# Kernel tuning notes

Hardware: AMD Instinct MI355X
Metric: run time of the kernel (lower is better)

## Reference

```python
import jax, jax.numpy as jnp
import numpy as np

BETA = 0.05
KNN = 6
UL_ALPHA = 0.05
UL_BETA = 1.0


def setup_inputs() -> dict:
    key = jax.random.key(0)
    k1, k2, k3 = jax.random.split(key, 3)
    B, D, N = 256, 2048, 16384
    inputs = jax.random.normal(k1, (B, D), dtype=jnp.float32)
    em = jax.random.normal(k2, (N, D), dtype=jnp.float32)
    # exemplar memory rows are kept unit-norm by the update rule
    em = em / jnp.linalg.norm(em, axis=1, keepdims=True)
    targets = jax.random.randint(k3, (B,), 0, N, dtype=jnp.int64)
    return {"inputs": inputs, "em": em, "targets": targets, "epoch": 10}


def smooth_hot(logits, targets, em, k):
    # Vectorized k-reciprocal neighbor search (replaces the per-sample Python loop).
    m, n = logits.shape
    # index_sorted[:, :k] == top-k class indices per sample
    _, topk_idx = jax.lax.top_k(logits, k)            # [m, k]
    neigh = em[topk_idx]                               # [m, k, d]
    sims = jnp.einsum('mkd,nd->mkn', neigh, em)        # [m, k, n]
    _, neigh_topk = jax.lax.top_k(sims, k)             # [m, k, k]
    # neighbor j of sample i is reciprocal if anchor (top-1 of i) is in its top-k
    anchor = topk_idx[:, :1, None]                     # [m, 1, 1]
    recip = (neigh_topk == anchor).any(axis=-1)        # [m, k]
    weights = jnp.where(recip, 3.0 / k, 0.0).astype(logits.dtype)
    rows = jnp.arange(m)[:, None]
    onehot = jnp.zeros_like(logits).at[rows, topk_idx].set(weights)
    onehot = onehot.at[jnp.arange(m), targets].set(1.0)
    return onehot


def reference(inputs, em, targets, epoch):
    # ExemplarMemory.forward: similarity logits against the memory bank
    logits = (inputs @ em.T) / BETA                    # [B, N]
    # epoch >= 5 and knn > 0 branch (epoch=10)
    onehot = jax.lax.stop_gradient(
        smooth_hot(jax.lax.stop_gradient(logits), targets, em, KNN))
    logp = jax.nn.log_softmax(logits, axis=1)
    beta_loss = (-(onehot * logp).sum(axis=1)).mean()
    t_re = jnp.where(onehot == 0.0, jnp.float32(1e-4), onehot)
    alpha_loss = (-(jax.nn.softmax(logits, axis=1) * jnp.log(t_re)).sum(axis=1)).mean()
    return (UL_ALPHA * alpha_loss, UL_BETA * beta_loss)
```

## Files before the change

kernel.cpp:

```cpp
#include <hip/hip_runtime.h>
#include <math.h>

#define DIMK 2048
#define NEMB 16384
#define NB 256
#define NR2 1536
#define INV_BETA 20.0f
#define NEG_INF (-3.0e38f)

typedef short short8 __attribute__((ext_vector_type(8)));
typedef float f32x4 __attribute__((ext_vector_type(4)));
typedef const __attribute__((address_space(1))) unsigned int* gas_ptr;
typedef __attribute__((address_space(3))) unsigned int* las_ptr;

__device__ __forceinline__ void gl_lds16(const void* g, void* l) {
  __builtin_amdgcn_global_load_lds((gas_ptr)g, (las_ptr)l, 16, 0, 0);
}

__device__ __forceinline__ unsigned short f2bf(float f) {
  unsigned u = __float_as_uint(f);
  u += 0x7fffu + ((u >> 16) & 1u);
  return (unsigned short)(u >> 16);
}

__device__ __forceinline__ void ins6i(float x, int xi, float v[6], int vi[6]) {
  if (x > v[5] || (x == v[5] && xi < vi[5])) {
    v[5] = x; vi[5] = xi;
#pragma unroll
    for (int j = 5; j > 0; j--) {
      if (v[j] > v[j - 1] || (v[j] == v[j - 1] && vi[j] < vi[j - 1])) {
        float tv = v[j]; v[j] = v[j - 1]; v[j - 1] = tv;
        int ti = vi[j]; vi[j] = vi[j - 1]; vi[j - 1] = ti;
      }
    }
  }
}

__global__ __launch_bounds__(256) void cvt_kernel(const float* __restrict__ src,
                                                  unsigned short* __restrict__ dst, int n4) {
  int i = blockIdx.x * 256 + threadIdx.x;
  if (i < n4) {
    float4 f = ((const float4*)src)[i];
    ushort4 o;
    o.x = f2bf(f.x); o.y = f2bf(f.y); o.z = f2bf(f.z); o.w = f2bf(f.w);
    ((ushort4*)dst)[i] = o;
  }
}

template <int MODE>
__global__ __launch_bounds__(256, 4) void gemm_kernel(
    const unsigned short* __restrict__ Abase, const unsigned short* __restrict__ Bbase,
    const int* __restrict__ nidx, float* __restrict__ outC,
    const float* __restrict__ saIn, int* __restrict__ cntOut) {
  constexpr int MTILE = (MODE == 0) ? 64 : 128;
  constexpr int MI = 4;
  constexpr int NI = (MODE == 0) ? 2 : 4;
  constexpr int NSUB_A = MTILE / 16;
  constexpr int NSUB = NSUB_A + 8;
  constexpr int NA = NSUB / 4;
  constexpr int NK = DIMK / 32;

  __shared__ unsigned short st[3][NSUB * 512];
  __shared__ int rowIdxSh[128];
  __shared__ float saSh[128];
  __shared__ int cntSh[128];
  int t = threadIdx.x;
  int lane = t & 63, wave = t >> 6;
  int quad = lane >> 4, l16 = lane & 15;
  int wr = (MODE == 0) ? 0 : (wave >> 1);
  int wc = (MODE == 0) ? wave : (wave & 1);
  int bn = blockIdx.x, bm = blockIdx.y;

  if constexpr (MODE == 1) {
    if (t < 128) {
      rowIdxSh[t] = nidx[bm * 128 + t];
      saSh[t] = saIn[bm * 128 + t];
      cntSh[t] = 0;
    }
  }
  __syncthreads();

  const unsigned short* agp[NA];
  int soff[NA];
  {
    int seg = lane >> 4;
#pragma unroll
    for (int a = 0; a < NA; a++) {
      int s = wave + a * 4;
      const unsigned short* basep;
      size_t goff;
      if (s < NSUB_A) {
        int r = s * 16 + l16;
        int grow = (MODE == 0) ? (bm * MTILE + r) : rowIdxSh[r];
        basep = Abase;
        goff = (size_t)grow * DIMK;
      } else {
        int r = (s - NSUB_A) * 16 + l16;
        basep = Bbase;
        goff = (size_t)(bn * 128 + r) * DIMK;
      }
      agp[a] = basep + goff + seg * 8;
      soff[a] = s * 512;
    }
  }

  f32x4 acc[MI][NI];
#pragma unroll
  for (int mi = 0; mi < MI; mi++)
#pragma unroll
    for (int ni = 0; ni < NI; ni++) acc[mi][ni] = (f32x4)0.0f;

  int lo = lane * 8;

#pragma unroll
  for (int p = 0; p < 3; p++)
#pragma unroll
    for (int a = 0; a < NA; a++) gl_lds16(agp[a] + p * 32, &st[p][soff[a]]);

  int cur = 0;
  for (int k = 0; k < NK; k++) {
    if (k < NK - 2) {
      if constexpr (MODE == 0) asm volatile("s_waitcnt vmcnt(6)" ::: "memory");
      else                     asm volatile("s_waitcnt vmcnt(8)" ::: "memory");
    } else if (k == NK - 2) {
      if constexpr (MODE == 0) asm volatile("s_waitcnt vmcnt(3)" ::: "memory");
      else                     asm volatile("s_waitcnt vmcnt(4)" ::: "memory");
    } else {
      asm volatile("s_waitcnt vmcnt(0)" ::: "memory");
    }
    __builtin_amdgcn_s_barrier();
    asm volatile("" ::: "memory");

    const unsigned short* hb = &st[cur][0];
    short8 af[MI], bfv[NI];
#pragma unroll
    for (int mi = 0; mi < MI; mi++)
      af[mi] = *(const short8*)&hb[(wr * MI + mi) * 512 + lo];
#pragma unroll
    for (int ni = 0; ni < NI; ni++)
      bfv[ni] = *(const short8*)&hb[(NSUB_A + wc * NI + ni) * 512 + lo];

    asm volatile("s_waitcnt lgkmcnt(0)" ::: "memory");
    __builtin_amdgcn_s_barrier();
    asm volatile("" ::: "memory");

    if (k + 3 < NK) {
#pragma unroll
      for (int a = 0; a < NA; a++) gl_lds16(agp[a] + (k + 3) * 32, &st[cur][soff[a]]);
    }

#pragma unroll
    for (int mi = 0; mi < MI; mi++)
#pragma unroll
      for (int ni = 0; ni < NI; ni++)
        acc[mi][ni] =
            __builtin_amdgcn_mfma_f32_16x16x32_bf16(af[mi], bfv[ni], acc[mi][ni], 0, 0, 0);

    cur = (cur == 2) ? 0 : cur + 1;
  }

  if constexpr (MODE == 0) {
#pragma unroll
    for (int mi = 0; mi < MI; mi++) {
      int row = bm * MTILE + mi * 16 + quad * 4;
#pragma unroll
      for (int ni = 0; ni < NI; ni++) {
        int col = bn * 128 + wave * 32 + ni * 16 + l16;
#pragma unroll
        for (int rr = 0; rr < 4; rr++)
          outC[(size_t)(row + rr) * NEMB + col] = acc[mi][ni][rr] * INV_BETA;
      }
    }
  } else {
#pragma unroll
    for (int mi = 0; mi < MI; mi++) {
#pragma unroll
      for (int rr = 0; rr < 4; rr++) {
        int rloc = wr * 64 + mi * 16 + quad * 4 + rr;
        float s = saSh[rloc];
        int c = 0;
#pragma unroll
        for (int ni = 0; ni < NI; ni++) c += (acc[mi][ni][rr] > s) ? 1 : 0;
        c += __shfl_xor(c, 1, 64);
        c += __shfl_xor(c, 2, 64);
        c += __shfl_xor(c, 4, 64);
        c += __shfl_xor(c, 8, 64);
        if (l16 == 0) atomicAdd(&cntSh[rloc], c);
      }
    }
    __syncthreads();
    if (t < 128) atomicAdd(&cntOut[bm * 128 + t], cntSh[t]);
  }
}

__global__ __launch_bounds__(1024) void rowstats_kernel(
    const float* __restrict__ logits, float* __restrict__ topv,
    int* __restrict__ topi, float* __restrict__ lse) {
  int m = blockIdx.x, t = threadIdx.x;
  const float4* row4 = (const float4*)(logits + (size_t)m * NEMB);
  float v6[6]; int i6[6];
#pragma unroll
  for (int j = 0; j < 6; j++) { v6[j] = NEG_INF; i6[j] = 0x7fffffff; }
  float vals[16];
#pragma unroll
  for (int j = 0; j < 4; j++) {
    float4 f = row4[t + j * 1024];
    vals[j * 4 + 0] = f.x; vals[j * 4 + 1] = f.y;
    vals[j * 4 + 2] = f.z; vals[j * 4 + 3] = f.w;
  }
  float mx = vals[0];
#pragma unroll
  for (int r = 1; r < 16; r++) mx = fmaxf(mx, vals[r]);
  float sme = 0.f;
#pragma unroll
  for (int r = 0; r < 16; r++) sme += expf(vals[r] - mx);
#pragma unroll
  for (int j = 0; j < 4; j++) {
    int base = (t + j * 1024) * 4;
#pragma unroll
    for (int b = 0; b < 4; b++) ins6i(vals[j * 4 + b], base + b, v6, i6);
  }
  __shared__ float sv[1024 * 6]; __shared__ int si[1024 * 6];
  __shared__ float smx[1024], ssm[1024];
#pragma unroll
  for (int j = 0; j < 6; j++) { sv[t * 6 + j] = v6[j]; si[t * 6 + j] = i6[j]; }
  smx[t] = mx; ssm[t] = sme;
  __syncthreads();
  for (int s = 512; s > 0; s >>= 1) {
    if (t < s) {
      float mo = smx[t + s], lo = ssm[t + s];
      float mn = fmaxf(smx[t], mo);
      ssm[t] = ssm[t] * expf(smx[t] - mn) + lo * expf(mo - mn);
      smx[t] = mn;
#pragma unroll
      for (int j = 0; j < 6; j++) ins6i(sv[(t + s) * 6 + j], si[(t + s) * 6 + j], v6, i6);
#pragma unroll
      for (int j = 0; j < 6; j++) { sv[t * 6 + j] = v6[j]; si[t * 6 + j] = i6[j]; }
    }
    __syncthreads();
  }
  if (t == 0) {
    lse[m] = smx[0] + logf(ssm[0]);
#pragma unroll
    for (int j = 0; j < 6; j++) { topv[m * 6 + j] = v6[j]; topi[m * 6 + j] = i6[j]; }
  }
}

__global__ __launch_bounds__(256) void sa_kernel(const float* __restrict__ em,
                                                 const int* __restrict__ topi,
                                                 float* __restrict__ sa,
                                                 int* __restrict__ cnt) {
  int gid = blockIdx.x * 256 + threadIdx.x;
  int w = gid >> 6, lane = gid & 63;
  if (w >= NR2) return;
  if (lane == 1) cnt[w] = 0;
  int m = w / 6;
  int i = topi[w], a = topi[m * 6];
  const float* ei = em + (size_t)i * DIMK;
  const float* ea = em + (size_t)a * DIMK;
  float s = 0.f;
  for (int d = lane; d < DIMK; d += 64) s += ei[d] * ea[d];
#pragma unroll
  for (int off = 32; off > 0; off >>= 1) s += __shfl_down(s, off, 64);
  if (lane == 0) sa[w] = s;
}

__global__ __launch_bounds__(256) void final_kernel(
    const float* __restrict__ logits, const float* __restrict__ topv,
    const int* __restrict__ topi, const float* __restrict__ lse_arr,
    const int* __restrict__ cnt, const int* __restrict__ targets,
    float* __restrict__ out) {
  int m = threadIdx.x;
  float lse = lse_arr[m];
  int tgt = targets[m];
  float tl = logits[(size_t)m * NEMB + tgt];
  float beta = 0.f, Ps = 0.f, nbp = 0.f;
  bool tin = false;
#pragma unroll
  for (int k = 0; k < 6; k++) {
    int idx = topi[m * 6 + k]; float v = topv[m * 6 + k];
    float p = expf(v - lse);
    if (idx == tgt) { tin = true; beta += (lse - v); Ps += p; }
    else if (cnt[m * 6 + k] < 6) { beta += 0.5f * (lse - v); Ps += p; nbp += p; }
  }
  if (!tin) { beta += (lse - tl); Ps += expf(tl - lse); }
  float alpha = 9.2103404f * (1.f - Ps) + 0.6931472f * nbp;
  __shared__ float sA[256], sB2[256];
  sA[m] = alpha; sB2[m] = beta;
  __syncthreads();
  for (int s = 128; s > 0; s >>= 1) {
    if (m < s) { sA[m] += sA[m + s]; sB2[m] += sB2[m + s]; }
    __syncthreads();
  }
  if (m == 0) { out[0] = 0.05f * sA[0] / 256.f; out[1] = sB2[0] / 256.f; }
}

extern "C" void kernel_launch(void* const* d_in, const int* in_sizes, int n_in,
                              void* d_out, int out_size, void* d_ws, size_t ws_size,
                              hipStream_t stream) {
  const float* x = (const float*)d_in[0];
  const float* em = (const float*)d_in[1];
  const int* targets = (const int*)d_in[2];
  char* ws = (char*)d_ws;
  unsigned short* em_bf = (unsigned short*)ws;
  unsigned short* x_bf  = (unsigned short*)(ws + 67108864);
  float* logits = (float*)(ws + 68157440);
  int*   cnt    = (int*)  (ws + 84934656);
  float* topv   = (float*)(ws + 89653248);
  int*   topi   = (int*)  (ws + 89659392);
  float* lse    = (float*)(ws + 89665536);
  float* sa     = (float*)(ws + 89666560);

  cvt_kernel<<<dim3(32768), dim3(256), 0, stream>>>(em, em_bf, NEMB * DIMK / 4);
  cvt_kernel<<<dim3(512), dim3(256), 0, stream>>>(x, x_bf, NB * DIMK / 4);
  gemm_kernel<0><<<dim3(128, 4), dim3(256), 0, stream>>>(x_bf, em_bf, (const int*)nullptr,
                                                         logits, (const float*)nullptr,
                                                         (int*)nullptr);
  rowstats_kernel<<<dim3(256), dim3(1024), 0, stream>>>(logits, topv, topi, lse);
  sa_kernel<<<dim3(384), dim3(256), 0, stream>>>(em, topi, sa, cnt);
  gemm_kernel<1><<<dim3(128, 12), dim3(256), 0, stream>>>(em_bf, em_bf, topi,
                                                          (float*)nullptr, sa, cnt);
  final_kernel<<<dim3(1), dim3(256), 0, stream>>>(logits, topv, topi, lse, cnt, targets,
                                                  (float*)d_out);
}
```

Measured before the change: 487.1 us.

## Split GEMM template and retile neighbor-count GEMM to 256-row, 512-thread blocks

Splits the templated GEMM into a plain logits GEMM and a dedicated neighbor-similarity counting GEMM. The counting GEMM now uses 512-thread blocks covering 256 gathered rows by 128 columns, with a K step of 64 split into two halves. It also uses hand-scheduled ds_read_b128 loads interleaved with MFMA groups, s_setprio around the MFMAs and sched barriers. The goal is more operand reuse per LDS byte and better overlap of LDS reads with matrix math. The cost is much larger shared memory (about 144KB per block), which caps occupancy, plus fragile manual wait counts.

Result: faster. 471.0 us (-3.3%).

```diff
diff --git a/kernel.cpp b/kernel.cpp
--- a/kernel.cpp
+++ b/kernel.cpp
@@ -16,6 +16,20 @@
 __device__ __forceinline__ void gl_lds16(const void* g, void* l) {
   __builtin_amdgcn_global_load_lds((gas_ptr)g, (las_ptr)l, 16, 0, 0);
 }
+
+__device__ __forceinline__ short8 dsr(const void* p) {
+  short8 r;
+  asm volatile("ds_read_b128 %0, %1"
+               : "=&v"(r)
+               : "v"((const __attribute__((address_space(3))) unsigned short*)p));
+  return r;
+}
+
+#define LGKM0_FENCE                                          \
+  do {                                                       \
+    asm volatile("s_waitcnt lgkmcnt(0)" ::: "memory");       \
+    __builtin_amdgcn_sched_barrier(0);                       \
+  } while (0)
 
 __device__ __forceinline__ unsigned short f2bf(float f) {
   unsigned u = __float_as_uint(f);
@@ -47,38 +61,16 @@
   }
 }
 
-template <int MODE>
-__global__ __launch_bounds__(256, 4) void gemm_kernel(
+__global__ __launch_bounds__(256, 4) void gemm0_kernel(
     const unsigned short* __restrict__ Abase, const unsigned short* __restrict__ Bbase,
-    const int* __restrict__ nidx, float* __restrict__ outC,
-    const float* __restrict__ saIn, int* __restrict__ cntOut) {
-  constexpr int MTILE = (MODE == 0) ? 64 : 128;
-  constexpr int MI = 4;
-  constexpr int NI = (MODE == 0) ? 2 : 4;
-  constexpr int NSUB_A = MTILE / 16;
-  constexpr int NSUB = NSUB_A + 8;
-  constexpr int NA = NSUB / 4;
-  constexpr int NK = DIMK / 32;
-
+    float* __restrict__ outC) {
+  constexpr int MI = 4, NI = 2, NSUB_A = 4, NSUB = 12, NA = 3, NK = DIMK / 32;
   __shared__ unsigned short st[3][NSUB * 512];
-  __shared__ int rowIdxSh[128];
-  __shared__ float saSh[128];
-  __shared__ int cntSh[128];
   int t = threadIdx.x;
   int lane = t & 63, wave = t >> 6;
   int quad = lane >> 4, l16 = lane & 15;
-  int wr = (MODE == 0) ? 0 : (wave >> 1);
-  int wc = (MODE == 0) ? wave : (wave & 1);
+  int wc = wave;
   int bn = blockIdx.x, bm = blockIdx.y;
-
-  if constexpr (MODE == 1) {
-    if (t < 128) {
-      rowIdxSh[t] = nidx[bm * 128 + t];
-      saSh[t] = saIn[bm * 128 + t];
-      cntSh[t] = 0;
-    }
-  }
-  __syncthreads();
 
   const unsigned short* agp[NA];
   int soff[NA];
@@ -87,17 +79,14 @@
 #pragma unroll
     for (int a = 0; a < NA; a++) {
       int s = wave + a * 4;
+      size_t goff;
       const unsigned short* basep;
-      size_t goff;
       if (s < NSUB_A) {
-        int r = s * 16 + l16;
-        int grow = (MODE == 0) ? (bm * MTILE + r) : rowIdxSh[r];
         basep = Abase;
-        goff = (size_t)grow * DIMK;
+        goff = (size_t)(bm * 64 + s * 16 + l16) * DIMK;
       } else {
-        int r = (s - NSUB_A) * 16 + l16;
         basep = Bbase;
-        goff = (size_t)(bn * 128 + r) * DIMK;
+        goff = (size_t)(bn * 128 + (s - NSUB_A) * 16 + l16) * DIMK;
       }
       agp[a] = basep + goff + seg * 8;
       soff[a] = s * 512;
@@ -111,7 +100,6 @@
     for (int ni = 0; ni < NI; ni++) acc[mi][ni] = (f32x4)0.0f;
 
   int lo = lane * 8;
-
 #pragma unroll
   for (int p = 0; p < 3; p++)
 #pragma unroll
@@ -119,78 +107,199 @@
 
   int cur = 0;
   for (int k = 0; k < NK; k++) {
-    if (k < NK - 2) {
-      if constexpr (MODE == 0) asm volatile("s_waitcnt vmcnt(6)" ::: "memory");
-      else                     asm volatile("s_waitcnt vmcnt(8)" ::: "memory");
-    } else if (k == NK - 2) {
-      if constexpr (MODE == 0) asm volatile("s_waitcnt vmcnt(3)" ::: "memory");
-      else                     asm volatile("s_waitcnt vmcnt(4)" ::: "memory");
-    } else {
-      asm volatile("s_waitcnt vmcnt(0)" ::: "memory");
-    }
+    if (k < NK - 2)      asm volatile("s_waitcnt vmcnt(6)" ::: "memory");
+    else if (k == NK - 2) asm volatile("s_waitcnt vmcnt(3)" ::: "memory");
+    else                 asm volatile("s_waitcnt vmcnt(0)" ::: "memory");
     __builtin_amdgcn_s_barrier();
     asm volatile("" ::: "memory");
-
     const unsigned short* hb = &st[cur][0];
     short8 af[MI], bfv[NI];
 #pragma unroll
-    for (int mi = 0; mi < MI; mi++)
-      af[mi] = *(const short8*)&hb[(wr * MI + mi) * 512 + lo];
+    for (int mi = 0; mi < MI; mi++) af[mi] = *(const short8*)&hb[mi * 512 + lo];
 #pragma unroll
     for (int ni = 0; ni < NI; ni++)
       bfv[ni] = *(const short8*)&hb[(NSUB_A + wc * NI + ni) * 512 + lo];
-
     asm volatile("s_waitcnt lgkmcnt(0)" ::: "memory");
     __builtin_amdgcn_s_barrier();
     asm volatile("" ::: "memory");
-
     if (k + 3 < NK) {
 #pragma unroll
       for (int a = 0; a < NA; a++) gl_lds16(agp[a] + (k + 3) * 32, &st[cur][soff[a]]);
     }
-
 #pragma unroll
     for (int mi = 0; mi < MI; mi++)
 #pragma unroll
       for (int ni = 0; ni < NI; ni++)
         acc[mi][ni] =
             __builtin_amdgcn_mfma_f32_16x16x32_bf16(af[mi], bfv[ni], acc[mi][ni], 0, 0, 0);
-
     cur = (cur == 2) ? 0 : cur + 1;
   }
 
-  if constexpr (MODE == 0) {
-#pragma unroll
-    for (int mi = 0; mi < MI; mi++) {
-      int row = bm * MTILE + mi * 16 + quad * 4;
-#pragma unroll
-      for (int ni = 0; ni < NI; ni++) {
-        int col = bn * 128 + wave * 32 + ni * 16 + l16;
-#pragma unroll
-        for (int rr = 0; rr < 4; rr++)
-          outC[(size_t)(row + rr) * NEMB + col] = acc[mi][ni][rr] * INV_BETA;
-      }
-    }
-  } else {
-#pragma unroll
-    for (int mi = 0; mi < MI; mi++) {
-#pragma unroll
-      for (int rr = 0; rr < 4; rr++) {
-        int rloc = wr * 64 + mi * 16 + quad * 4 + rr;
-        float s = saSh[rloc];
-        int c = 0;
-#pragma unroll
-        for (int ni = 0; ni < NI; ni++) c += (acc[mi][ni][rr] > s) ? 1 : 0;
-        c += __shfl_xor(c, 1, 64);
-        c += __shfl_xor(c, 2, 64);
-        c += __shfl_xor(c, 4, 64);
-        c += __shfl_xor(c, 8, 64);
-        if (l16 == 0) atomicAdd(&cntSh[rloc], c);
-      }
-    }
-    __syncthreads();
-    if (t < 128) atomicAdd(&cntOut[bm * 128 + t], cntSh[t]);
-  }
+#pragma unroll
+  for (int mi = 0; mi < MI; mi++) {
+    int row = bm * 64 + mi * 16 + quad * 4;
+#pragma unroll
+    for (int ni = 0; ni < NI; ni++) {
+      int col = bn * 128 + wave * 32 + ni * 16 + l16;
+#pragma unroll
+      for (int rr = 0; rr < 4; rr++)
+        outC[(size_t)(row + rr) * NEMB + col] = acc[mi][ni][rr] * INV_BETA;
+    }
+  }
+}
+
+__global__ __launch_bounds__(512, 2) void gemm1_kernel(
+    const unsigned short* __restrict__ em_bf, const int* __restrict__ nidx,
+    const float* __restrict__ saIn, int* __restrict__ cntOut) {
+  __shared__ unsigned short st[3][2][24 * 512];
+  __shared__ int rowIdxSh[256];
+  __shared__ float saSh[256];
+  __shared__ int cntSh[256];
+  int t = threadIdx.x;
+  int lane = t & 63, wave = t >> 6;
+  int quad = lane >> 4, l16 = lane & 15;
+  int wr = wave >> 2, wc = wave & 3;
+  int bn = blockIdx.x, bm = blockIdx.y;
+
+  if (t < 256) {
+    rowIdxSh[t] = nidx[bm * 256 + t];
+    saSh[t] = saIn[bm * 256 + t];
+    cntSh[t] = 0;
+  }
+  __syncthreads();
+
+  const unsigned short* agp[6];
+  unsigned ldsoff[6];
+  {
+    int seg = lane >> 4;
+#pragma unroll
+    for (int a = 0; a < 6; a++) {
+      int j = a % 3, h = a / 3;
+      int s = wave + j * 8;
+      size_t grow;
+      if (s < 16) grow = (size_t)rowIdxSh[s * 16 + l16];
+      else        grow = (size_t)(bn * 128 + (s - 16) * 16 + l16);
+      agp[a] = em_bf + grow * DIMK + h * 32 + seg * 8;
+      ldsoff[a] = (unsigned)(h * 24576 + s * 1024);
+    }
+  }
+
+  f32x4 acc[8][2];
+#pragma unroll
+  for (int mi = 0; mi < 8; mi++)
+#pragma unroll
+    for (int ni = 0; ni < 2; ni++) acc[mi][ni] = (f32x4)0.0f;
+
+  char* stb = (char*)&st[0][0][0];
+  unsigned aoffA = (unsigned)((wr * 8) * 1024 + lane * 16);
+  unsigned aoffB = (unsigned)((16 + wc * 2) * 1024 + lane * 16);
+
+#pragma unroll
+  for (int p = 0; p < 3; p++)
+#pragma unroll
+    for (int a = 0; a < 6; a++)
+      gl_lds16(agp[a] + p * 64, stb + p * 49152 + ldsoff[a]);
+
+  unsigned curoff = 0;
+  for (int k = 0; k < 32; k++) {
+    if (k < 30)       asm volatile("s_waitcnt vmcnt(12)" ::: "memory");
+    else if (k == 30) asm volatile("s_waitcnt vmcnt(6)" ::: "memory");
+    else              asm volatile("s_waitcnt vmcnt(0)" ::: "memory");
+    __builtin_amdgcn_s_barrier();
+    __builtin_amdgcn_sched_barrier(0);
+    const char* cb = stb + curoff;
+
+    short8 b00 = dsr(cb + aoffB);
+    short8 b10 = dsr(cb + aoffB + 1024);
+    short8 b01 = dsr(cb + aoffB + 24576);
+    short8 b11 = dsr(cb + aoffB + 25600);
+    short8 a00 = dsr(cb + aoffA);
+    short8 a01 = dsr(cb + aoffA + 24576);
+    short8 a10 = dsr(cb + aoffA + 1024);
+    short8 a11 = dsr(cb + aoffA + 25600);
+    LGKM0_FENCE;
+    short8 a20 = dsr(cb + aoffA + 2048);
+    short8 a21 = dsr(cb + aoffA + 26624);
+    short8 a30 = dsr(cb + aoffA + 3072);
+    short8 a31 = dsr(cb + aoffA + 27648);
+    __builtin_amdgcn_s_setprio(1);
+    acc[0][0] = __builtin_amdgcn_mfma_f32_16x16x32_bf16(a00, b00, acc[0][0], 0, 0, 0);
+    acc[0][0] = __builtin_amdgcn_mfma_f32_16x16x32_bf16(a01, b01, acc[0][0], 0, 0, 0);
+    acc[0][1] = __builtin_amdgcn_mfma_f32_16x16x32_bf16(a00, b10, acc[0][1], 0, 0, 0);
+    acc[0][1] = __builtin_amdgcn_mfma_f32_16x16x32_bf16(a01, b11, acc[0][1], 0, 0, 0);
+    acc[1][0] = __builtin_amdgcn_mfma_f32_16x16x32_bf16(a10, b00, acc[1][0], 0, 0, 0);
+    acc[1][0] = __builtin_amdgcn_mfma_f32_16x16x32_bf16(a11, b01, acc[1][0], 0, 0, 0);
+    acc[1][1] = __builtin_amdgcn_mfma_f32_16x16x32_bf16(a10, b10, acc[1][1], 0, 0, 0);
+    acc[1][1] = __builtin_amdgcn_mfma_f32_16x16x32_bf16(a11, b11, acc[1][1], 0, 0, 0);
+    __builtin_amdgcn_s_setprio(0);
+    LGKM0_FENCE;
+    short8 a40 = dsr(cb + aoffA + 4096);
+    short8 a41 = dsr(cb + aoffA + 28672);
+    short8 a50 = dsr(cb + aoffA + 5120);
+    short8 a51 = dsr(cb + aoffA + 29696);
+    __builtin_amdgcn_s_setprio(1);
+    acc[2][0] = __builtin_amdgcn_mfma_f32_16x16x32_bf16(a20, b00, acc[2][0], 0, 0, 0);
+    acc[2][0] = __builtin_amdgcn_mfma_f32_16x16x32_bf16(a21, b01, acc[2][0], 0, 0, 0);
+    acc[2][1] = __builtin_amdgcn_mfma_f32_16x16x32_bf16(a20, b10, acc[2][1], 0, 0, 0);
+    acc[2][1] = __builtin_amdgcn_mfma_f32_16x16x32_bf16(a21, b11, acc[2][1], 0, 0, 0);
+    acc[3][0] = __builtin_amdgcn_mfma_f32_16x16x32_bf16(a30, b00, acc[3][0], 0, 0, 0);
+    acc[3][0] = __builtin_amdgcn_mfma_f32_16x16x32_bf16(a31, b01, acc[3][0], 0, 0, 0);
+    acc[3][1] = __builtin_amdgcn_mfma_f32_16x16x32_bf16(a30, b10, acc[3][1], 0, 0, 0);
+    acc[3][1] = __builtin_amdgcn_mfma_f32_16x16x32_bf16(a31, b11, acc[3][1], 0, 0, 0);
+    __builtin_amdgcn_s_setprio(0);
+    LGKM0_FENCE;
+    short8 a60 = dsr(cb + aoffA + 6144);
+    short8 a61 = dsr(cb + aoffA + 30720);
+    short8 a70 = dsr(cb + aoffA + 7168);
+    short8 a71 = dsr(cb + aoffA + 31744);
+    __builtin_amdgcn_s_setprio(1);
+    acc[4][0] = __builtin_amdgcn_mfma_f32_16x16x32_bf16(a40, b00, acc[4][0], 0, 0, 0);
+    acc[4][0] = __builtin_amdgcn_mfma_f32_16x16x32_bf16(a41, b01, acc[4][0], 0, 0, 0);
+    acc[4][1] = __builtin_amdgcn_mfma_f32_16x16x32_bf16(a40, b10, acc[4][1], 0, 0, 0);
+    acc[4][1] = __builtin_amdgcn_mfma_f32_16x16x32_bf16(a41, b11, acc[4][1], 0, 0, 0);
+    acc[5][0] = __builtin_amdgcn_mfma_f32_16x16x32_bf16(a50, b00, acc[5][0], 0, 0, 0);
+    acc[5][0] = __builtin_amdgcn_mfma_f32_16x16x32_bf16(a51, b01, acc[5][0], 0, 0, 0);
+    acc[5][1] = __builtin_amdgcn_mfma_f32_16x16x32_bf16(a50, b10, acc[5][1], 0, 0, 0);
+    acc[5][1] = __builtin_amdgcn_mfma_f32_16x16x32_bf16(a51, b11, acc[5][1], 0, 0, 0);
+    __builtin_amdgcn_s_setprio(0);
+    LGKM0_FENCE;
+    __builtin_amdgcn_s_barrier();
+    __builtin_amdgcn_sched_barrier(0);
+    if (k < 29) {
+      char* sb = stb + curoff;
+#pragma unroll
+      for (int a = 0; a < 6; a++)
+        gl_lds16(agp[a] + (size_t)(k + 3) * 64, sb + ldsoff[a]);
+    }
+    __builtin_amdgcn_s_setprio(1);
+    acc[6][0] = __builtin_amdgcn_mfma_f32_16x16x32_bf16(a60, b00, acc[6][0], 0, 0, 0);
+    acc[6][0] = __builtin_amdgcn_mfma_f32_16x16x32_bf16(a61, b01, acc[6][0], 0, 0, 0);
+    acc[6][1] = __builtin_amdgcn_mfma_f32_16x16x32_bf16(a60, b10, acc[6][1], 0, 0, 0);
+    acc[6][1] = __builtin_amdgcn_mfma_f32_16x16x32_bf16(a61, b11, acc[6][1], 0, 0, 0);
+    acc[7][0] = __builtin_amdgcn_mfma_f32_16x16x32_bf16(a70, b00, acc[7][0], 0, 0, 0);
+    acc[7][0] = __builtin_amdgcn_mfma_f32_16x16x32_bf16(a71, b01, acc[7][0], 0, 0, 0);
+    acc[7][1] = __builtin_amdgcn_mfma_f32_16x16x32_bf16(a70, b10, acc[7][1], 0, 0, 0);
+    acc[7][1] = __builtin_amdgcn_mfma_f32_16x16x32_bf16(a71, b11, acc[7][1], 0, 0, 0);
+    __builtin_amdgcn_s_setprio(0);
+    curoff = (curoff == 98304u) ? 0u : curoff + 49152u;
+  }
+
+#pragma unroll
+  for (int mi = 0; mi < 8; mi++) {
+#pragma unroll
+    for (int rr = 0; rr < 4; rr++) {
+      int rloc = wr * 128 + mi * 16 + quad * 4 + rr;
+      float s = saSh[rloc];
+      int c = ((acc[mi][0][rr] > s) ? 1 : 0) + ((acc[mi][1][rr] > s) ? 1 : 0);
+      c += __shfl_xor(c, 1, 64);
+      c += __shfl_xor(c, 2, 64);
+      c += __shfl_xor(c, 4, 64);
+      c += __shfl_xor(c, 8, 64);
+      if (l16 == 0) atomicAdd(&cntSh[rloc], c);
+    }
+  }
+  __syncthreads();
+  if (t < 256) atomicAdd(&cntOut[bm * 256 + t], cntSh[t]);
 }
 
 __global__ __launch_bounds__(1024) void rowstats_kernel(
@@ -313,13 +422,10 @@
 
   cvt_kernel<<<dim3(32768), dim3(256), 0, stream>>>(em, em_bf, NEMB * DIMK / 4);
   cvt_kernel<<<dim3(512), dim3(256), 0, stream>>>(x, x_bf, NB * DIMK / 4);
-  gemm_kernel<0><<<dim3(128, 4), dim3(256), 0, stream>>>(x_bf, em_bf, (const int*)nullptr,
-                                                         logits, (const float*)nullptr,
-                                                         (int*)nullptr);
+  gemm0_kernel<<<dim3(128, 4), dim3(256), 0, stream>>>(x_bf, em_bf, logits);
   rowstats_kernel<<<dim3(256), dim3(1024), 0, stream>>>(logits, topv, topi, lse);
   sa_kernel<<<dim3(384), dim3(256), 0, stream>>>(em, topi, sa, cnt);
-  gemm_kernel<1><<<dim3(128, 12), dim3(256), 0, stream>>>(em_bf, em_bf, topi,
-                                                          (float*)nullptr, sa, cnt);
+  gemm1_kernel<<<dim3(128, 6), dim3(512), 0, stream>>>(em_bf, topi, sa, cnt);
   final_kernel<<<dim3(1), dim3(256), 0, stream>>>(logits, topv, topi, lse, cnt, targets,
                                                   (float*)d_out);
 }
```
